# Kernel tuning notes

Measured on AMD Instinct MI355X. Metric: run time of the kernel, lower is better.

Reference implementation:

```python
import jax, jax.numpy as jnp
import numpy as np

D_MODEL = 2048
D_INNER = 4096
D_CONV = 4
D_STATE = 16
DT_RANK = 128  # (d_model + 15) // 16
EPS = 1e-5
B_SZ, SEQ = 2, 2048


def _silu(x):
    return x * jax.nn.sigmoid(x)


def setup_inputs() -> dict:
    key = jax.random.key(0)
    ks = jax.random.split(key, 10)
    s = lambda k, shape, sc=0.02: jax.random.normal(k, shape, jnp.float32) * sc
    # S4D-real init for A_log, small negative bias for dt (standard Mamba init)
    A_log = jnp.log(jnp.tile(jnp.arange(1, D_STATE + 1, dtype=jnp.float32), (D_INNER, 1)))
    return {
        "hidden_states": jax.random.normal(ks[0], (B_SZ, SEQ, D_MODEL), jnp.float32),
        "norm_scale": jnp.ones((D_MODEL,), jnp.float32),
        "in_proj_w": s(ks[1], (2 * D_INNER, D_MODEL)),
        "conv_w": s(ks[2], (D_INNER, 1, D_CONV), 0.1),
        "conv_b": s(ks[3], (D_INNER,), 0.1),
        "x_proj_w": s(ks[4], (DT_RANK + 2 * D_STATE, D_INNER)),
        "dt_proj_w": s(ks[5], (D_INNER, DT_RANK), 0.1),
        "dt_proj_b": jnp.full((D_INNER,), -4.0, jnp.float32) + s(ks[6], (D_INNER,), 0.1),
        "out_proj_w": s(ks[7], (D_MODEL, D_INNER)),
        "A_log": A_log,
        "D": jnp.ones((D_INNER,), jnp.float32),
    }


def reference(hidden_states, norm_scale, in_proj_w, conv_w, conv_b, x_proj_w,
              dt_proj_w, dt_proj_b, out_proj_w, A_log, D):
    B, L, _ = hidden_states.shape
    residual = hidden_states
    # RMSNorm
    rms = jnp.sqrt(jnp.mean(hidden_states ** 2, axis=-1, keepdims=True) + EPS)
    xn = hidden_states / rms * norm_scale
    # in_proj -> [B, L, 2*d_inner]; torch code keeps this as projected_states
    xz = jnp.einsum('bld,ed->ble', xn, in_proj_w)
    x_in = xz[..., :D_INNER].transpose(0, 2, 1)  # [B, d_inner, L]
    z = xz[..., D_INNER:]                        # [B, L, d_inner]
    # depthwise causal conv1d (padding d_conv-1, truncated to L) + SiLU
    xc = jax.lax.conv_general_dilated(
        x_in, conv_w, window_strides=(1,), padding=[(D_CONV - 1, 0)],
        feature_group_count=D_INNER)
    xc = _silu(xc + conv_b[None, :, None])       # [B, d_inner, L]
    # x_proj -> dt, B, C
    x_dbl = jnp.einsum('bdl,rd->brl', xc, x_proj_w)  # [B, dt_rank+2*d_state, L]
    dt_low = x_dbl[:, :DT_RANK]
    Bm = x_dbl[:, DT_RANK:DT_RANK + D_STATE]         # [B, d_state, L]
    Cm = x_dbl[:, DT_RANK + D_STATE:]                # [B, d_state, L]
    delta = jax.nn.softplus(
        jnp.einsum('dr,brl->bdl', dt_proj_w, dt_low) + dt_proj_b[None, :, None])
    A = -jnp.exp(A_log)                              # [d_inner, d_state]
    # selective scan: h_t = exp(delta_t * A) * h_{t-1} + delta_t * B_t * u_t
    delta_t = delta.transpose(2, 0, 1)  # [L, B, d_inner]
    u_t = xc.transpose(2, 0, 1)         # [L, B, d_inner]
    B_t = Bm.transpose(2, 0, 1)         # [L, B, d_state]
    C_t = Cm.transpose(2, 0, 1)         # [L, B, d_state]

    def step(h, inp):
        d_, b_, c_, u_ = inp
        dA = jnp.exp(d_[..., None] * A)                      # [B, d_inner, d_state]
        h = h * dA + (d_ * u_)[..., None] * b_[:, None, :]   # [B, d_inner, d_state]
        y = jnp.einsum('bds,bs->bd', h, c_)                  # [B, d_inner]
        return h, y

    h0 = jnp.zeros((B, D_INNER, D_STATE), hidden_states.dtype)
    _, ys = jax.lax.scan(step, h0, (delta_t, B_t, C_t, u_t))  # [L, B, d_inner]
    y = ys.transpose(1, 0, 2) + xc.transpose(0, 2, 1) * D     # [B, L, d_inner]
    y = y * _silu(z)
    out = jnp.einsum('bld,od->blo', y, out_proj_w)            # [B, L, d_model]
    return residual + out, xz
```

## Files before the change

### kernel.cpp

```cpp
#include <hip/hip_runtime.h>
#include <cstdint>
#include <cstddef>

#define DM   2048
#define DI   4096
#define DST  16
#define DTR  128
#define SEQL 2048
#define NTOK 4096
#define XZW  8192
#define NCHAIN 8192
#define CL   64
#define NCH  32

typedef short short8 __attribute__((ext_vector_type(8)));
typedef float f32x4 __attribute__((ext_vector_type(4)));

__device__ __forceinline__ short f2bf(float x) {
  union { float f; uint32_t u; } v; v.f = x;
  uint32_t r = v.u + 0x7fffu + ((v.u >> 16) & 1u);
  return (short)(r >> 16);
}
__device__ __forceinline__ float bf2f(short s) {
  union { uint32_t u; float f; } v; v.u = ((uint32_t)(uint16_t)s) << 16;
  return v.f;
}

__device__ __forceinline__ void stage16(const short* g, short* l) {
#if __has_builtin(__builtin_amdgcn_global_load_lds)
  __builtin_amdgcn_global_load_lds((const __attribute__((address_space(1))) void*)g,
                                   (__attribute__((address_space(3))) void*)l, 16, 0, 0);
#else
  *(short8*)l = *(const short8*)g;
#endif
}

__global__ __launch_bounds__(256) void cvt4_k(const float* __restrict__ in,
                                              short* __restrict__ out, int n4) {
  int i = blockIdx.x * 256 + threadIdx.x;
  if (i >= n4) return;
  float4 v = ((const float4*)in)[i];
  short4 o;
  o.x = f2bf(v.x); o.y = f2bf(v.y); o.z = f2bf(v.z); o.w = f2bf(v.w);
  ((short4*)out)[i] = o;
}

__global__ __launch_bounds__(256) void pad_xproj_k(const float* __restrict__ xp,
                                                   short* __restrict__ out) {
  int i = blockIdx.x * 256 + threadIdx.x;
  if (i >= 256 * 1024) return;
  int r = i >> 10;
  float4 v = make_float4(0.f, 0.f, 0.f, 0.f);
  if (r < 160) v = ((const float4*)xp)[i];
  short4 o;
  o.x = f2bf(v.x); o.y = f2bf(v.y); o.z = f2bf(v.z); o.w = f2bf(v.w);
  ((short4*)out)[i] = o;
}

__global__ __launch_bounds__(256) void rmsnorm_k(const float* __restrict__ hs,
                                                 const float* __restrict__ sc,
                                                 short* __restrict__ xn) {
  const int token = blockIdx.x;
  const int tid = threadIdx.x;
  const float* row = hs + (size_t)token * DM;
  float4 a = ((const float4*)row)[tid];
  float4 b = ((const float4*)row)[tid + 256];
  float ss = a.x*a.x + a.y*a.y + a.z*a.z + a.w*a.w
           + b.x*b.x + b.y*b.y + b.z*b.z + b.w*b.w;
  #pragma unroll
  for (int o = 32; o > 0; o >>= 1) ss += __shfl_xor(ss, o);
  __shared__ float wsum[4];
  if ((tid & 63) == 0) wsum[tid >> 6] = ss;
  __syncthreads();
  float tot = wsum[0] + wsum[1] + wsum[2] + wsum[3];
  float inv = rsqrtf(tot * (1.0f / DM) + 1e-5f);
  float4 s1 = ((const float4*)sc)[tid];
  float4 s2 = ((const float4*)sc)[tid + 256];
  short4 o1, o2;
  o1.x = f2bf(a.x * inv * s1.x); o1.y = f2bf(a.y * inv * s1.y);
  o1.z = f2bf(a.z * inv * s1.z); o1.w = f2bf(a.w * inv * s1.w);
  o2.x = f2bf(b.x * inv * s2.x); o2.y = f2bf(b.y * inv * s2.y);
  o2.z = f2bf(b.z * inv * s2.z); o2.w = f2bf(b.w * inv * s2.w);
  ((short4*)xn)[(size_t)token * (DM / 4) + tid] = o1;
  ((short4*)xn)[(size_t)token * (DM / 4) + tid + 256] = o2;
}

template <int MFR, int EPI>
__global__ __launch_bounds__(512) void gemm_big(const short* __restrict__ A,
                                                const short* __restrict__ B,
                                                int K, int N, int nbx,
                                                float* __restrict__ out_f,
                                                const float* __restrict__ aux_f) {
  constexpr int BM = MFR * 32;
  constexpr int ABYTES = BM * 128;
  constexpr int BBYTES = 256 * 128;
  constexpr int AINSTR = ABYTES / 8192;
  constexpr int BUF = ABYTES + BBYTES;
  __shared__ char lds[2 * BUF];

  const int tid = threadIdx.x;
  const int lane = tid & 63;
  const int wid = tid >> 6;
  const int wm = wid >> 2;
  const int wn = wid & 3;
  const int lr = lane & 15;
  const int lj = lane >> 4;

  const int nwg = gridDim.x;
  const int wg = blockIdx.x;
  const int swz = (wg & 7) * (nwg >> 3) + (wg >> 3);
  const int bx = swz % nbx;
  const int by = swz / nbx;
  const size_t m0 = (size_t)by * BM;
  const size_t n0 = (size_t)bx * 256;

  const int NT = K >> 6;

  auto stA = [&](int t, char* buf) {
    const int k0 = t << 6;
    #pragma unroll
    for (int s = 0; s < AINSTR; ++s) {
      const int off = s * 8192 + tid * 16;
      const int r = off >> 7;
      const int j = (off >> 4) & 7;
      stage16(A + (m0 + r) * (size_t)K + k0 + ((j ^ (r & 7)) << 3),
              (short*)(buf + off));
    }
  };
  auto stB = [&](int t, char* buf) {
    const int k0 = t << 6;
    #pragma unroll
    for (int s = 0; s < 4; ++s) {
      const int off = s * 8192 + tid * 16;
      const int r = off >> 7;
      const int j = (off >> 4) & 7;
      stage16(B + (n0 + r) * (size_t)K + k0 + ((j ^ (r & 7)) << 3),
              (short*)(buf + ABYTES + off));
    }
  };

  f32x4 acc[MFR][4] = {};

  stA(0, lds);
  stB(0, lds);

  for (int t = 0; t < NT; ++t) {
    char* cur = lds + (t & 1) * BUF;
    char* nxt = lds + ((t + 1) & 1) * BUF;
    const bool more = (t + 1) < NT;
    if (more) {
      stA(t + 1, nxt);
      stB(t + 1, nxt);
      if constexpr (AINSTR == 4) asm volatile("s_waitcnt vmcnt(8)" ::: "memory");
      else                       asm volatile("s_waitcnt vmcnt(6)" ::: "memory");
    } else {
      asm volatile("s_waitcnt vmcnt(0)" ::: "memory");
    }
    __builtin_amdgcn_s_barrier();
    __builtin_amdgcn_sched_barrier(0);
    #pragma unroll
    for (int q = 0; q < 4; ++q) {
      short8 av[MFR / 2][2];
      short8 bv[2][2];
      #pragma unroll
      for (int f = 0; f < MFR / 2; ++f) {
        const int arow = wm * (BM / 2) + ((q >> 1) * (MFR / 2) + f) * 16 + lr;
        #pragma unroll
        for (int ks = 0; ks < 2; ++ks)
          av[f][ks] = *(const short8*)(cur + arow * 128 +
                        ((((ks << 2) + lj) ^ (arow & 7)) << 4));
      }
      #pragma unroll
      for (int g = 0; g < 2; ++g) {
        const int brow = wn * 64 + ((q & 1) * 2 + g) * 16 + lr;
        #pragma unroll
        for (int ks = 0; ks < 2; ++ks)
          bv[g][ks] = *(const short8*)(cur + ABYTES + brow * 128 +
                        ((((ks << 2) + lj) ^ (brow & 7)) << 4));
      }
      __builtin_amdgcn_s_setprio(1);
      #pragma unroll
      for (int f = 0; f < MFR / 2; ++f)
        #pragma unroll
        for (int g = 0; g < 2; ++g)
          #pragma unroll
          for (int ks = 0; ks < 2; ++ks) {
            f32x4& a = acc[(q >> 1) * (MFR / 2) + f][(q & 1) * 2 + g];
            a = __builtin_amdgcn_mfma_f32_16x16x32_bf16(av[f][ks], bv[g][ks], a, 0, 0, 0);
          }
      __builtin_amdgcn_s_setprio(0);
    }
    __builtin_amdgcn_s_barrier();
  }

  #pragma unroll
  for (int f = 0; f < MFR; ++f)
    #pragma unroll
    for (int g = 0; g < 4; ++g)
      #pragma unroll
      for (int jj = 0; jj < 4; ++jj) {
        const size_t row = m0 + wm * (BM / 2) + f * 16 + lj * 4 + jj;
        const size_t col = n0 + wn * 64 + g * 16 + lr;
        float v = acc[f][g][jj];
        if constexpr (EPI == 3) v += aux_f[row * (size_t)N + col];
        out_f[row * (size_t)N + col] = v;
      }
}

template <int EPI>
__global__ __launch_bounds__(256) void gemm_nt(const short* __restrict__ A,
                                               const short* __restrict__ B,
                                               int K, int N,
                                               const float* __restrict__ aux_f,
                                               short* __restrict__ out_bf,
                                               float* __restrict__ outB,
                                               float* __restrict__ outC) {
  __shared__ short As[128 * 64];
  __shared__ short Bs[128 * 64];
  const int tid = threadIdx.x;
  const int lane = tid & 63;
  const int wid = tid >> 6;
  const int wr = wid >> 1, wc = wid & 1;
  const size_t m0 = (size_t)blockIdx.y * 128;
  const size_t n0 = (size_t)blockIdx.x * 128;
  f32x4 acc[4][4] = {};
  for (int k0 = 0; k0 < K; k0 += 64) {
    #pragma unroll
    for (int i = 0; i < 4; ++i) {
      const int off = i * 4096 + tid * 16;
      const int r = off >> 7;
      const int ke = (off & 127) >> 1;
      stage16(A + (m0 + r) * K + k0 + ke, &As[off >> 1]);
      stage16(B + (n0 + r) * K + k0 + ke, &Bs[off >> 1]);
    }
    __syncthreads();
    #pragma unroll
    for (int kk = 0; kk < 64; kk += 32) {
      short8 af[4], bfr[4];
      const int kb = kk + (lane >> 4) * 8;
      const int rr = lane & 15;
      #pragma unroll
      for (int f = 0; f < 4; ++f) {
        af[f]  = *(const short8*)&As[(wr * 64 + f * 16 + rr) * 64 + kb];
        bfr[f] = *(const short8*)&Bs[(wc * 64 + f * 16 + rr) * 64 + kb];
      }
      #pragma unroll
      for (int fm = 0; fm < 4; ++fm)
        #pragma unroll
        for (int fn = 0; fn < 4; ++fn)
          acc[fm][fn] = __builtin_amdgcn_mfma_f32_16x16x32_bf16(af[fm], bfr[fn], acc[fm][fn], 0, 0, 0);
    }
    __syncthreads();
  }
  const int rbase = (lane >> 4) * 4;
  const int cbase = lane & 15;
  #pragma unroll
  for (int fm = 0; fm < 4; ++fm) {
    #pragma unroll
    for (int fn = 0; fn < 4; ++fn) {
      #pragma unroll
      for (int j = 0; j < 4; ++j) {
        const size_t row = m0 + wr * 64 + fm * 16 + rbase + j;
        const size_t col = n0 + wc * 64 + fn * 16 + cbase;
        const float v = acc[fm][fn][j];
        if constexpr (EPI == 1) {
          if (col < 128)      out_bf[row * 128 + col] = f2bf(v);
          else if (col < 144) outB[row * 16 + (col - 128)] = v;
          else if (col < 160) outC[row * 16 + (col - 144)] = v;
        } else {
          float x = v + aux_f[col];
          float sp = (x > 20.f) ? x : log1pf(__expf(x));
          out_bf[row * (size_t)N + col] = f2bf(sp);
        }
      }
    }
  }
}

__global__ __launch_bounds__(256) void conv_silu_k(const float* __restrict__ xz,
                                                   const float* __restrict__ cw,
                                                   const float* __restrict__ cb,
                                                   short* __restrict__ xc) {
  const int d = blockIdx.x * 256 + threadIdx.x;
  const int t0 = blockIdx.y * 8;
  const int l0 = t0 & (SEQL - 1);
  const float4 w = ((const float4*)cw)[d];
  const float bias = cb[d];
  float x0 = (l0 >= 3) ? xz[(size_t)(t0 - 3) * XZW + d] : 0.f;
  float x1 = (l0 >= 2) ? xz[(size_t)(t0 - 2) * XZW + d] : 0.f;
  float x2 = (l0 >= 1) ? xz[(size_t)(t0 - 1) * XZW + d] : 0.f;
  #pragma unroll
  for (int i = 0; i < 8; ++i) {
    const float x3 = xz[(size_t)(t0 + i) * XZW + d];
    const float acc = bias + w.x * x0 + w.y * x1 + w.z * x2 + w.w * x3;
    const float sv = acc / (1.f + __expf(-acc));
    xc[(size_t)(t0 + i) * DI + d] = f2bf(sv);
    x0 = x1; x1 = x2; x2 = x3;
  }
}

__global__ __launch_bounds__(256) void scan1_k(const short* __restrict__ del_bf,
                                               const short* __restrict__ xc,
                                               const float* __restrict__ Bc,
                                               const float* __restrict__ alog,
                                               float* __restrict__ hloc,
                                               float* __restrict__ Ssum) {
  const int t = blockIdx.x * 256 + threadIdx.x;
  const int sub = t & 3;
  const int chain = (t >> 2) & (NCHAIN - 1);
  const int chunk = t >> 15;
  const int b = chain >> 12;
  const int d = chain & 4095;
  float A[4];
  #pragma unroll
  for (int j = 0; j < 4; ++j) A[j] = -__expf(alog[d * 16 + sub * 4 + j]);
  float h0 = 0.f, h1 = 0.f, h2 = 0.f, h3 = 0.f, S = 0.f;
  size_t token = (size_t)b * SEQL + (size_t)chunk * CL;
  for (int l = 0; l < CL; ++l, ++token) {
    const float delta = bf2f(del_bf[token * DI + d]);
    const float u = bf2f(xc[token * DI + d]);
    const float du = delta * u;
    S += delta;
    const float4 Bv = ((const float4*)Bc)[token * 4 + sub];
    h0 = h0 * __expf(delta * A[0]) + du * Bv.x;
    h1 = h1 * __expf(delta * A[1]) + du * Bv.y;
    h2 = h2 * __expf(delta * A[2]) + du * Bv.z;
    h3 = h3 * __expf(delta * A[3]) + du * Bv.w;
  }
  ((float4*)hloc)[(size_t)(chunk * NCHAIN + chain) * 4 + sub] =
      make_float4(h0, h1, h2, h3);
  if (sub == 0) Ssum[chunk * NCHAIN + chain] = S;
}

__global__ __launch_bounds__(256) void scan2_k(const float* __restrict__ hloc,
                                               const float* __restrict__ Ssum,
                                               const float* __restrict__ alog,
                                               float* __restrict__ hin) {
  const int t = blockIdx.x * 256 + threadIdx.x;
  const int sub = t & 3;
  const int chain = t >> 2;
  const int d = chain & 4095;
  float A[4];
  #pragma unroll
  for (int j = 0; j < 4; ++j) A[j] = -__expf(alog[d * 16 + sub * 4 + j]);
  float4 h = make_float4(0.f, 0.f, 0.f, 0.f);
  for (int c = 0; c < NCH; ++c) {
    const size_t idx = (size_t)(c * NCHAIN + chain) * 4 + sub;
    ((float4*)hin)[idx] = h;
    const float S = Ssum[c * NCHAIN + chain];
    const float4 hl = ((const float4*)hloc)[idx];
    h.x = h.x * __expf(A[0] * S) + hl.x;
    h.y = h.y * __expf(A[1] * S) + hl.y;
    h.z = h.z * __expf(A[2] * S) + hl.z;
    h.w = h.w * __expf(A[3] * S) + hl.w;
  }
}

__global__ __launch_bounds__(256) void scan3_k(const short* __restrict__ del_bf,
                                               const short* __restrict__ xc,
                                               const float* __restrict__ Bc,
                                               const float* __restrict__ Cc,
                                               const float* __restrict__ xzbuf,
                                               const float* __restrict__ alog,
                                               const float* __restrict__ dvec,
                                               const float* __restrict__ hin,
                                               short* __restrict__ y) {
  const int t = blockIdx.x * 256 + threadIdx.x;
  const int sub = t & 3;
  const int chain = (t >> 2) & (NCHAIN - 1);
  const int chunk = t >> 15;
  const int b = chain >> 12;
  const int d = chain & 4095;
  float A[4];
  #pragma unroll
  for (int j = 0; j < 4; ++j) A[j] = -__expf(alog[d * 16 + sub * 4 + j]);
  const float Dd = dvec[d];
  float4 h = ((const float4*)hin)[(size_t)(chunk * NCHAIN + chain) * 4 + sub];
  size_t token = (size_t)b * SEQL + (size_t)chunk * CL;
  for (int l = 0; l < CL; ++l, ++token) {
    const float delta = bf2f(del_bf[token * DI + d]);
    const float u = bf2f(xc[token * DI + d]);
    const float du = delta * u;
    const float4 Bv = ((const float4*)Bc)[token * 4 + sub];
    const float4 Cv = ((const float4*)Cc)[token * 4 + sub];
    h.x = h.x * __expf(delta * A[0]) + du * Bv.x;
    h.y = h.y * __expf(delta * A[1]) + du * Bv.y;
    h.z = h.z * __expf(delta * A[2]) + du * Bv.z;
    h.w = h.w * __expf(delta * A[3]) + du * Bv.w;
    float yp = h.x * Cv.x + h.y * Cv.y + h.z * Cv.z + h.w * Cv.w;
    yp += __shfl_xor(yp, 1);
    yp += __shfl_xor(yp, 2);
    if (sub == 0) {
      const float z = xzbuf[token * XZW + DI + d];
      const float sz = z / (1.f + __expf(-z));
      y[token * DI + d] = f2bf((yp + u * Dd) * sz);
    }
  }
}

extern "C" void kernel_launch(void* const* d_in, const int* in_sizes, int n_in,
                              void* d_out, int out_size, void* d_ws, size_t ws_size,
                              hipStream_t stream) {
  const float* hs   = (const float*)d_in[0];
  const float* nsc  = (const float*)d_in[1];
  const float* win  = (const float*)d_in[2];
  const float* cw   = (const float*)d_in[3];
  const float* cb   = (const float*)d_in[4];
  const float* wxp  = (const float*)d_in[5];
  const float* wdt  = (const float*)d_in[6];
  const float* bdt  = (const float*)d_in[7];
  const float* wout = (const float*)d_in[8];
  const float* alog = (const float*)d_in[9];
  const float* dvec = (const float*)d_in[10];

  float* out0 = (float*)d_out;
  float* xz   = out0 + (size_t)NTOK * DM;

  char* w = (char*)d_ws;
  size_t off = 0;
  auto alloc = [&](size_t bytes) {
    char* p = w + off;
    off += (bytes + 255) & ~(size_t)255;
    return p;
  };
  short* xn_bf   = (short*)alloc((size_t)NTOK * DM * 2);
  short* win_bf  = (short*)alloc((size_t)XZW * DM * 2);
  short* wout_bf = (short*)alloc((size_t)DM * DI * 2);
  short* wdt_bf  = (short*)alloc((size_t)DI * DTR * 2);
  short* wxp_bf  = (short*)alloc((size_t)256 * DI * 2);
  short* xc_bf   = (short*)alloc((size_t)NTOK * DI * 2);
  short* dtl_bf  = (short*)alloc((size_t)NTOK * DTR * 2);
  float* Bc      = (float*)alloc((size_t)NTOK * DST * 4);
  float* Cc      = (float*)alloc((size_t)NTOK * DST * 4);
  short* del_bf  = (short*)alloc((size_t)NTOK * DI * 2);
  short* y_bf    = (short*)alloc((size_t)NTOK * DI * 2);

  float* hloc = (float*)win_bf;
  float* hin  = (float*)((char*)win_bf + (size_t)NCH * NCHAIN * DST * 4);
  float* Ssum = (float*)xn_bf;

  cvt4_k<<<16384, 256, 0, stream>>>(win,  win_bf,  (XZW * DM) / 4);
  cvt4_k<<<8192,  256, 0, stream>>>(wout, wout_bf, (DM * DI) / 4);
  cvt4_k<<<512,   256, 0, stream>>>(wdt,  wdt_bf,  (DI * DTR) / 4);
  pad_xproj_k<<<1024, 256, 0, stream>>>(wxp, wxp_bf);

  rmsnorm_k<<<NTOK, 256, 0, stream>>>(hs, nsc, xn_bf);
  gemm_big<8, 0><<<dim3((XZW / 256) * (NTOK / 256)), 512, 0, stream>>>(
      xn_bf, win_bf, DM, XZW, XZW / 256, xz, nullptr);
  conv_silu_k<<<dim3(DI / 256, NTOK / 8), 256, 0, stream>>>(xz, cw, cb, xc_bf);
  gemm_nt<1><<<dim3(2, NTOK / 128), 256, 0, stream>>>(
      xc_bf, wxp_bf, DI, 256, nullptr, dtl_bf, Bc, Cc);
  gemm_nt<2><<<dim3(DI / 128, NTOK / 128), 256, 0, stream>>>(
      dtl_bf, wdt_bf, DTR, DI, bdt, del_bf, nullptr, nullptr);
  scan1_k<<<(NCHAIN * 4 * NCH) / 256, 256, 0, stream>>>(
      del_bf, xc_bf, Bc, alog, hloc, Ssum);
  scan2_k<<<(NCHAIN * 4) / 256, 256, 0, stream>>>(hloc, Ssum, alog, hin);
  scan3_k<<<(NCHAIN * 4 * NCH) / 256, 256, 0, stream>>>(
      del_bf, xc_bf, Bc, Cc, xz, alog, dvec, hin, y_bf);
  gemm_big<4, 3><<<dim3((DM / 256) * (NTOK / 128)), 512, 0, stream>>>(
      y_bf, wout_bf, DI, DM, DM / 256, out0, hs);
}
```

Before: 665.3 us.

## Split-K the x_proj GEMM and rebalance chunked scan with 8 states per thread

```diff
diff --git a/kernel.cpp b/kernel.cpp
--- a/kernel.cpp
+++ b/kernel.cpp
@@ -10,8 +10,8 @@
 #define NTOK 4096
 #define XZW  8192
 #define NCHAIN 8192
-#define CL   64
-#define NCH  32
+#define CL   32
+#define NCH  64
 
 typedef short short8 __attribute__((ext_vector_type(8)));
 typedef float f32x4 __attribute__((ext_vector_type(4)));
@@ -210,11 +210,10 @@
 template <int EPI>
 __global__ __launch_bounds__(256) void gemm_nt(const short* __restrict__ A,
                                                const short* __restrict__ B,
-                                               int K, int N,
+                                               int ld, int K, int N,
+                                               float* __restrict__ out_f,
                                                const float* __restrict__ aux_f,
-                                               short* __restrict__ out_bf,
-                                               float* __restrict__ outB,
-                                               float* __restrict__ outC) {
+                                               short* __restrict__ out_bf) {
   __shared__ short As[128 * 64];
   __shared__ short Bs[128 * 64];
   const int tid = threadIdx.x;
@@ -223,6 +222,8 @@
   const int wr = wid >> 1, wc = wid & 1;
   const size_t m0 = (size_t)blockIdx.y * 128;
   const size_t n0 = (size_t)blockIdx.x * 128;
+  A += (size_t)blockIdx.z * K;
+  B += (size_t)blockIdx.z * K;
   f32x4 acc[4][4] = {};
   for (int k0 = 0; k0 < K; k0 += 64) {
     #pragma unroll
@@ -230,8 +231,8 @@
       const int off = i * 4096 + tid * 16;
       const int r = off >> 7;
       const int ke = (off & 127) >> 1;
-      stage16(A + (m0 + r) * K + k0 + ke, &As[off >> 1]);
-      stage16(B + (n0 + r) * K + k0 + ke, &Bs[off >> 1]);
+      stage16(A + (m0 + r) * (size_t)ld + k0 + ke, &As[off >> 1]);
+      stage16(B + (n0 + r) * (size_t)ld + k0 + ke, &Bs[off >> 1]);
     }
     __syncthreads();
     #pragma unroll
@@ -263,18 +264,31 @@
         const size_t row = m0 + wr * 64 + fm * 16 + rbase + j;
         const size_t col = n0 + wc * 64 + fn * 16 + cbase;
         const float v = acc[fm][fn][j];
-        if constexpr (EPI == 1) {
-          if (col < 128)      out_bf[row * 128 + col] = f2bf(v);
-          else if (col < 144) outB[row * 16 + (col - 128)] = v;
-          else if (col < 160) outC[row * 16 + (col - 144)] = v;
-        } else {
+        if constexpr (EPI == 2) {
           float x = v + aux_f[col];
           float sp = (x > 20.f) ? x : log1pf(__expf(x));
           out_bf[row * (size_t)N + col] = f2bf(sp);
+        } else {
+          out_f[((size_t)blockIdx.z * NTOK + row) * (size_t)N + col] = v;
         }
       }
     }
   }
+}
+
+__global__ __launch_bounds__(256) void xdbl_epi_k(const float* __restrict__ part,
+                                                  short* __restrict__ dtl,
+                                                  float* __restrict__ Bc,
+                                                  float* __restrict__ Cc) {
+  const int row = blockIdx.x;
+  const int col = threadIdx.x;
+  const size_t i = (size_t)row * 256 + col;
+  const float v = part[i] + part[(size_t)NTOK * 256 + i]
+                + part[(size_t)2 * NTOK * 256 + i]
+                + part[(size_t)3 * NTOK * 256 + i];
+  if (col < 128)      dtl[(size_t)row * 128 + col] = f2bf(v);
+  else if (col < 144) Bc[(size_t)row * 16 + (col - 128)] = v;
+  else if (col < 160) Cc[(size_t)row * 16 + (col - 144)] = v;
 }
 
 __global__ __launch_bounds__(256) void conv_silu_k(const float* __restrict__ xz,
@@ -306,49 +320,52 @@
                                                float* __restrict__ hloc,
                                                float* __restrict__ Ssum) {
   const int t = blockIdx.x * 256 + threadIdx.x;
-  const int sub = t & 3;
-  const int chain = (t >> 2) & (NCHAIN - 1);
-  const int chunk = t >> 15;
+  const int sub = t & 1;
+  const int chain = (t >> 1) & (NCHAIN - 1);
+  const int chunk = t >> 14;
   const int b = chain >> 12;
   const int d = chain & 4095;
-  float A[4];
-  #pragma unroll
-  for (int j = 0; j < 4; ++j) A[j] = -__expf(alog[d * 16 + sub * 4 + j]);
-  float h0 = 0.f, h1 = 0.f, h2 = 0.f, h3 = 0.f, S = 0.f;
+  float A[8];
+  #pragma unroll
+  for (int j = 0; j < 8; ++j) A[j] = -__expf(alog[d * 16 + sub * 8 + j]);
+  float h[8] = {};
+  float S = 0.f;
   size_t token = (size_t)b * SEQL + (size_t)chunk * CL;
+  #pragma unroll 2
   for (int l = 0; l < CL; ++l, ++token) {
     const float delta = bf2f(del_bf[token * DI + d]);
     const float u = bf2f(xc[token * DI + d]);
     const float du = delta * u;
     S += delta;
-    const float4 Bv = ((const float4*)Bc)[token * 4 + sub];
-    h0 = h0 * __expf(delta * A[0]) + du * Bv.x;
-    h1 = h1 * __expf(delta * A[1]) + du * Bv.y;
-    h2 = h2 * __expf(delta * A[2]) + du * Bv.z;
-    h3 = h3 * __expf(delta * A[3]) + du * Bv.w;
-  }
-  ((float4*)hloc)[(size_t)(chunk * NCHAIN + chain) * 4 + sub] =
-      make_float4(h0, h1, h2, h3);
+    const float4 B0 = ((const float4*)Bc)[token * 4 + sub * 2];
+    const float4 B1 = ((const float4*)Bc)[token * 4 + sub * 2 + 1];
+    const float Bv[8] = {B0.x, B0.y, B0.z, B0.w, B1.x, B1.y, B1.z, B1.w};
+    #pragma unroll
+    for (int j = 0; j < 8; ++j)
+      h[j] = h[j] * __expf(delta * A[j]) + du * Bv[j];
+  }
+  const size_t idx = (size_t)(chunk * NCHAIN + chain) * 4 + sub * 2;
+  ((float4*)hloc)[idx]     = make_float4(h[0], h[1], h[2], h[3]);
+  ((float4*)hloc)[idx + 1] = make_float4(h[4], h[5], h[6], h[7]);
   if (sub == 0) Ssum[chunk * NCHAIN + chain] = S;
 }
 
-__global__ __launch_bounds__(256) void scan2_k(const float* __restrict__ hloc,
+__global__ __launch_bounds__(256) void scan2_k(float* __restrict__ hloc,
                                                const float* __restrict__ Ssum,
-                                               const float* __restrict__ alog,
-                                               float* __restrict__ hin) {
+                                               const float* __restrict__ alog) {
   const int t = blockIdx.x * 256 + threadIdx.x;
-  const int sub = t & 3;
+  const int q = t & 3;
   const int chain = t >> 2;
   const int d = chain & 4095;
   float A[4];
   #pragma unroll
-  for (int j = 0; j < 4; ++j) A[j] = -__expf(alog[d * 16 + sub * 4 + j]);
+  for (int j = 0; j < 4; ++j) A[j] = -__expf(alog[d * 16 + q * 4 + j]);
   float4 h = make_float4(0.f, 0.f, 0.f, 0.f);
   for (int c = 0; c < NCH; ++c) {
-    const size_t idx = (size_t)(c * NCHAIN + chain) * 4 + sub;
-    ((float4*)hin)[idx] = h;
+    const size_t idx = (size_t)(c * NCHAIN + chain) * 4 + q;
     const float S = Ssum[c * NCHAIN + chain];
     const float4 hl = ((const float4*)hloc)[idx];
+    ((float4*)hloc)[idx] = h;
     h.x = h.x * __expf(A[0] * S) + hl.x;
     h.y = h.y * __expf(A[1] * S) + hl.y;
     h.z = h.z * __expf(A[2] * S) + hl.z;
@@ -366,30 +383,38 @@
                                                const float* __restrict__ hin,
                                                short* __restrict__ y) {
   const int t = blockIdx.x * 256 + threadIdx.x;
-  const int sub = t & 3;
-  const int chain = (t >> 2) & (NCHAIN - 1);
-  const int chunk = t >> 15;
+  const int sub = t & 1;
+  const int chain = (t >> 1) & (NCHAIN - 1);
+  const int chunk = t >> 14;
   const int b = chain >> 12;
   const int d = chain & 4095;
-  float A[4];
-  #pragma unroll
-  for (int j = 0; j < 4; ++j) A[j] = -__expf(alog[d * 16 + sub * 4 + j]);
+  float A[8];
+  #pragma unroll
+  for (int j = 0; j < 8; ++j) A[j] = -__expf(alog[d * 16 + sub * 8 + j]);
   const float Dd = dvec[d];
-  float4 h = ((const float4*)hin)[(size_t)(chunk * NCHAIN + chain) * 4 + sub];
+  const size_t idx = (size_t)(chunk * NCHAIN + chain) * 4 + sub * 2;
+  const float4 h0 = ((const float4*)hin)[idx];
+  const float4 h1 = ((const float4*)hin)[idx + 1];
+  float h[8] = {h0.x, h0.y, h0.z, h0.w, h1.x, h1.y, h1.z, h1.w};
   size_t token = (size_t)b * SEQL + (size_t)chunk * CL;
+  #pragma unroll 2
   for (int l = 0; l < CL; ++l, ++token) {
     const float delta = bf2f(del_bf[token * DI + d]);
     const float u = bf2f(xc[token * DI + d]);
     const float du = delta * u;
-    const float4 Bv = ((const float4*)Bc)[token * 4 + sub];
-    const float4 Cv = ((const float4*)Cc)[token * 4 + sub];
-    h.x = h.x * __expf(delta * A[0]) + du * Bv.x;
-    h.y = h.y * __expf(delta * A[1]) + du * Bv.y;
-    h.z = h.z * __expf(delta * A[2]) + du * Bv.z;
-    h.w = h.w * __expf(delta * A[3]) + du * Bv.w;
-    float yp = h.x * Cv.x + h.y * Cv.y + h.z * Cv.z + h.w * Cv.w;
+    const float4 B0 = ((const float4*)Bc)[token * 4 + sub * 2];
+    const float4 B1 = ((const float4*)Bc)[token * 4 + sub * 2 + 1];
+    const float4 C0 = ((const float4*)Cc)[token * 4 + sub * 2];
+    const float4 C1 = ((const float4*)Cc)[token * 4 + sub * 2 + 1];
+    const float Bv[8] = {B0.x, B0.y, B0.z, B0.w, B1.x, B1.y, B1.z, B1.w};
+    const float Cv[8] = {C0.x, C0.y, C0.z, C0.w, C1.x, C1.y, C1.z, C1.w};
+    float yp = 0.f;
+    #pragma unroll
+    for (int j = 0; j < 8; ++j) {
+      h[j] = h[j] * __expf(delta * A[j]) + du * Bv[j];
+      yp += h[j] * Cv[j];
+    }
     yp += __shfl_xor(yp, 1);
-    yp += __shfl_xor(yp, 2);
     if (sub == 0) {
       const float z = xzbuf[token * XZW + DI + d];
       const float sz = z / (1.f + __expf(-z));
@@ -435,9 +460,9 @@
   short* del_bf  = (short*)alloc((size_t)NTOK * DI * 2);
   short* y_bf    = (short*)alloc((size_t)NTOK * DI * 2);
 
-  float* hloc = (float*)win_bf;
-  float* hin  = (float*)((char*)win_bf + (size_t)NCH * NCHAIN * DST * 4);
-  float* Ssum = (float*)xn_bf;
+  float* xp_part = (float*)win_bf;
+  float* hloc    = (float*)win_bf;
+  float* Ssum    = (float*)xn_bf;
 
   cvt4_k<<<16384, 256, 0, stream>>>(win,  win_bf,  (XZW * DM) / 4);
   cvt4_k<<<8192,  256, 0, stream>>>(wout, wout_bf, (DM * DI) / 4);
@@ -448,15 +473,16 @@
   gemm_big<8, 0><<<dim3((XZW / 256) * (NTOK / 256)), 512, 0, stream>>>(
       xn_bf, win_bf, DM, XZW, XZW / 256, xz, nullptr);
   conv_silu_k<<<dim3(DI / 256, NTOK / 8), 256, 0, stream>>>(xz, cw, cb, xc_bf);
-  gemm_nt<1><<<dim3(2, NTOK / 128), 256, 0, stream>>>(
-      xc_bf, wxp_bf, DI, 256, nullptr, dtl_bf, Bc, Cc);
-  gemm_nt<2><<<dim3(DI / 128, NTOK / 128), 256, 0, stream>>>(
-      dtl_bf, wdt_bf, DTR, DI, bdt, del_bf, nullptr, nullptr);
-  scan1_k<<<(NCHAIN * 4 * NCH) / 256, 256, 0, stream>>>(
+  gemm_nt<4><<<dim3(2, NTOK / 128, 4), 256, 0, stream>>>(
+      xc_bf, wxp_bf, DI, DI / 4, 256, xp_part, nullptr, nullptr);
+  xdbl_epi_k<<<NTOK, 256, 0, stream>>>(xp_part, dtl_bf, Bc, Cc);
+  gemm_nt<2><<<dim3(DI / 128, NTOK / 128, 1), 256, 0, stream>>>(
+      dtl_bf, wdt_bf, DTR, DTR, DI, nullptr, bdt, del_bf);
+  scan1_k<<<(NCHAIN * 2 * NCH) / 256, 256, 0, stream>>>(
       del_bf, xc_bf, Bc, alog, hloc, Ssum);
-  scan2_k<<<(NCHAIN * 4) / 256, 256, 0, stream>>>(hloc, Ssum, alog, hin);
-  scan3_k<<<(NCHAIN * 4 * NCH) / 256, 256, 0, stream>>>(
-      del_bf, xc_bf, Bc, Cc, xz, alog, dvec, hin, y_bf);
+  scan2_k<<<(NCHAIN * 4) / 256, 256, 0, stream>>>(hloc, Ssum, alog);
+  scan3_k<<<(NCHAIN * 2 * NCH) / 256, 256, 0, stream>>>(
+      del_bf, xc_bf, Bc, Cc, xz, alog, dvec, hloc, y_bf);
   gemm_big<4, 3><<<dim3((DM / 256) * (NTOK / 128)), 512, 0, stream>>>(
       y_bf, wout_bf, DI, DM, DM / 256, out0, hs);
 }
```

New measurement: 581.3 us. 1.14x faster.
